# Kernel optimization log

Measured on AMD Instinct MI355X. Metric: run time of the kernel, lower is better.

Reference implementation:

```python
import math
import jax, jax.numpy as jnp
import numpy as np

T, B, IN, H, D, ETA, R = 128, 32, 512, 8, 64, 4, 4
DE = ETA * D  # expanded key dim = eta * head_dim
EPS = 1e-05


def setup_inputs() -> dict:
    key = jax.random.key(0)
    ks = jax.random.split(key, 8)
    s = 0.05
    return {
        "inputs": jax.random.normal(ks[0], (T, B, IN), jnp.float32),
        "terminations": jnp.zeros((T, B), jnp.float32),
        "tilde_k_prev": jax.random.normal(ks[1], (B, R, H, DE), jnp.float32) * s,
        "tilde_v_prev": jax.random.normal(ks[2], (B, R, H, D), jnp.float32) * s,
        "s_prev": jax.random.normal(ks[3], (B, H, DE), jnp.float32) * s,
        "tick": jnp.zeros((B, 1), jnp.float32),
        "W_kqv": jax.random.normal(ks[4], (H * D * 5, IN), jnp.float32) * s,
        "b_kqv": jnp.zeros((H * D * 5,), jnp.float32),
        "W_p": jax.random.normal(ks[5], (H * ETA * 3, IN), jnp.float32) * s,
        "b_p": jnp.zeros((H * ETA * 3,), jnp.float32),
        "W_o": jax.random.normal(ks[6], (IN, H * D), jnp.float32) * s,
        "b_o": jnp.zeros((IN,), jnp.float32),
    }


def _forward(inputs, terminations, tilde_k_prev, tilde_v_prev, s_prev, tick,
             W_kqv, b_kqv, W_p, b_p, W_o, b_o):
    # projections
    kqv = (inputs @ W_kqv.T + b_kqv).reshape(T, B, H, 5, D)
    keys, queries, values, beta, gammas = (kqv[..., i, :] for i in range(5))
    p = (inputs @ W_p.T + b_p).reshape(T, B, H, 3, ETA)
    p1, p2, p3 = (p[..., i, :] for i in range(3))
    relu, sig = jax.nn.relu, jax.nn.sigmoid
    # kernel feature maps: outer product then flatten (d outer, n inner)
    keys = jnp.einsum('tbhd,tbhn->tbhdn', relu(keys), relu(p1)).reshape(T, B, H, DE)
    queries = jnp.einsum('tbhd,tbhn->tbhdn', relu(queries), relu(p2)).reshape(T, B, H, DE)
    gammas = jnp.einsum('tbhd,tbhn->tbhdn', sig(gammas), sig(p3)).reshape(T, B, H, DE)
    beta = sig(beta)  # (T,B,H,D)
    # oscillatory basis
    ticks = tick[None] + jnp.arange(1, T + 1, dtype=jnp.float32).reshape(T, 1, 1)  # (T,B,1)
    omegas = jnp.linspace(-math.pi, math.pi, R)
    occil = jnp.cos(ticks * omegas[None, None, :])  # (T,B,R)
    values = values * beta
    values_r = values[:, :, None] * occil[:, :, :, None, None]   # (T,B,R,H,D)
    keys_g = keys * gammas                                        # (T,B,H,DE)
    keys_r = keys_g[:, :, None] * occil[:, :, :, None, None]     # (T,B,R,H,DE)
    # discounts (with termination resets)
    nt = (1.0 - terminations)[:, :, None, None]
    dg = (1.0 - gammas) * nt  # (T,B,H,DE)
    db = (1.0 - beta) * nt    # (T,B,H,D)
    # recurrence y[t] = discount[t]*y[t-1] + x[t] via lax.scan over T
    def step(carry, xs):
        k_st, v_st, s_st = carry
        kx, vx, sx, dgt, dbt = xs
        k_new = dgt[:, None] * k_st + kx   # (B,R,H,DE)
        v_new = dbt[:, None] * v_st + vx   # (B,R,H,D)
        s_new = dgt * s_st + sx            # (B,H,DE)
        return (k_new, v_new, s_new), (k_new, v_new, s_new)
    (kf, vf, sf), (K, V, S) = jax.lax.scan(
        step, (tilde_k_prev, tilde_v_prev, s_prev), (keys_r, values_r, keys_g, dg, db))
    # attention readout
    kdq = jnp.einsum('tbrhd,tbhd->tbrh', K, queries)
    kv = jnp.einsum('tbrhd,tbrh->tbhd', V, kdq)
    norm = jnp.einsum('tbhd,tbhd->tbh', S, queries)
    attn = kv / (2 * R * norm[..., None] + EPS)  # (T,B,H,D)
    out = attn.reshape(T, B, H * D) @ W_o.T + b_o  # dropout p=0 (eval)
    return out, kf, vf, sf, tick + T


def reference(inputs, terminations, tilde_k_prev, tilde_v_prev, s_prev, tick,
              W_kqv, b_kqv, W_p, b_p, W_o, b_o):
    return _forward(inputs, terminations, tilde_k_prev, tilde_v_prev, s_prev, tick,
                    W_kqv, b_kqv, W_p, b_p, W_o, b_o)
```

## Files before the change

kernel.cpp:

```cpp
#include <hip/hip_runtime.h>
#include <math.h>
#include <stdint.h>

constexpr int T_ = 128, B_ = 32, IN_ = 512, H_ = 8, D_ = 64, ETA_ = 4, R_ = 4;
constexpr int DE_ = ETA_ * D_;
constexpr float EPS_ = 1e-5f;
constexpr int M_   = T_ * B_;
constexpr int BH_  = B_ * H_;
constexpr int NC2  = 16;
constexpr int CH2  = T_ / NC2;

constexpr int NW = 2688;
constexpr int SPLITCOL = 1664;

typedef __attribute__((ext_vector_type(8))) short bf16x8;
typedef __attribute__((ext_vector_type(4))) float f32x4;

__device__ __forceinline__ float bf2f(unsigned short u) {
    return __builtin_bit_cast(float, ((unsigned)u) << 16);
}
__device__ __forceinline__ unsigned short f2bf(float f) {
    unsigned u = __builtin_bit_cast(unsigned, f);
    u = (u + 0x7fffu + ((u >> 16) & 1u)) >> 16;
    return (unsigned short)u;
}
__device__ __forceinline__ float fsigm(float x) {
    return __fdividef(1.f, 1.f + __expf(-x));
}

constexpr int N4A = M_ * 128;
constexpr int N4W = NW * 128;
constexpr int N8O = IN_ * IN_ / 8;
constexpr int NPREP = N4A + N4W + N8O;

__global__ __launch_bounds__(256) void prep_all(
    const float* __restrict__ inputs,
    const float* __restrict__ Wkqv, const float* __restrict__ Wp,
    const float* __restrict__ bkqv, const float* __restrict__ bp,
    const float* __restrict__ Wo,
    unsigned short* __restrict__ A2, unsigned short* __restrict__ W2,
    float* __restrict__ bias_perm, unsigned short* __restrict__ Wo_bf)
{
    int i = blockIdx.x * 256 + threadIdx.x;
    if (i < N4A) {
        const int r = i >> 7;
        const int c = (i & 127) << 2;
        float4 x = *(const float4*)(inputs + (size_t)r * 512 + c);
        ushort4 hi = make_ushort4(f2bf(x.x), f2bf(x.y), f2bf(x.z), f2bf(x.w));
        ushort4 lo = make_ushort4(f2bf(x.x - bf2f(hi.x)), f2bf(x.y - bf2f(hi.y)),
                                  f2bf(x.z - bf2f(hi.z)), f2bf(x.w - bf2f(hi.w)));
        unsigned short* dr = A2 + (size_t)r * 1024 + c;
        *(ushort4*)dr = hi;
        *(ushort4*)(dr + 512) = lo;
        return;
    }
    i -= N4A;
    if (i < N4W) {
        const int rr = i >> 7;
        const int c = (i & 127) << 2;
        bool zero = false;
        const float* srow = nullptr;
        float bv = 0.f;
        if (rr < 512) {
            const int h = rr >> 6, dd = rr & 63, s = h * 320 + dd;
            srow = Wkqv + (size_t)s * 512; bv = bkqv[s];
        } else if (rr < 1024) {
            const int q = rr - 512, h = q >> 6, dd = q & 63, s = h * 320 + 64 + dd;
            srow = Wkqv + (size_t)s * 512; bv = bkqv[s];
        } else if (rr < 1536) {
            const int q = rr - 1024, h = q >> 6, dd = q & 63, s = h * 320 + 256 + dd;
            srow = Wkqv + (size_t)s * 512; bv = bkqv[s];
        } else if (rr < 1632) {
            const int q = rr - 1536;
            srow = Wp + (size_t)q * 512; bv = bp[q];
        } else if (rr < 1664) {
            zero = true;
        } else if (rr < 2176) {
            const int q = rr - 1664, h = q >> 6, dd = q & 63, s = h * 320 + 128 + dd;
            srow = Wkqv + (size_t)s * 512; bv = bkqv[s];
        } else {
            const int q = rr - 2176, h = q >> 6, dd = q & 63, s = h * 320 + 192 + dd;
            srow = Wkqv + (size_t)s * 512; bv = bkqv[s];
        }
        float4 x = zero ? make_float4(0.f, 0.f, 0.f, 0.f) : *(const float4*)(srow + c);
        ushort4 hi = make_ushort4(f2bf(x.x), f2bf(x.y), f2bf(x.z), f2bf(x.w));
        ushort4 lo = make_ushort4(f2bf(x.x - bf2f(hi.x)), f2bf(x.y - bf2f(hi.y)),
                                  f2bf(x.z - bf2f(hi.z)), f2bf(x.w - bf2f(hi.w)));
        unsigned short* dr = W2 + (size_t)rr * 1536 + c;
        *(ushort4*)dr = hi;
        *(ushort4*)(dr + 512) = lo;
        *(ushort4*)(dr + 1024) = hi;
        if (c == 0) bias_perm[rr] = zero ? 0.f : bv;
        return;
    }
    i -= N4W;
    if (i < N8O) {
        const float4* s = (const float4*)Wo;
        float4 a = s[2 * i], b = s[2 * i + 1];
        *(ushort4*)(Wo_bf + 8 * i)     = make_ushort4(f2bf(a.x), f2bf(a.y), f2bf(a.z), f2bf(a.w));
        *(ushort4*)(Wo_bf + 8 * i + 4) = make_ushort4(f2bf(b.x), f2bf(b.y), f2bf(b.z), f2bf(b.w));
    }
}

__device__ __forceinline__ void gl_lds16(const unsigned short* g, unsigned short* l) {
    __builtin_amdgcn_global_load_lds((const __attribute__((address_space(1))) void*)g,
                                     (__attribute__((address_space(3))) void*)l, 16, 0, 0);
}

template <int BM, int BN>
__global__ __launch_bounds__(256) void gemm_bf16(
    const unsigned short* __restrict__ A,
    const unsigned short* __restrict__ W,
    const float* __restrict__ bias,
    float* __restrict__ C,
    int N, int sA, int sW, int kBig, int kSmall, int splitcol)
{
    constexpr int WM = BM / 2, WN = BN / 2;
    constexpr int AM = WM / 16, AN = WN / 16;
    constexpr int NLA = BM / 64;
    constexpr int NLB = BN / 64;
    constexpr int NLD = NLA + NLB;

    int bx, by;
    {
        const int nwg = gridDim.x * gridDim.y;
        int lin = blockIdx.y * gridDim.x + blockIdx.x;
        lin = (lin & 7) * (nwg >> 3) + (lin >> 3);
        const int G = (gridDim.x % 7 == 0) ? 7 : gridDim.x;
        const int grpsz = gridDim.y * G;
        const int cg = lin / grpsz, rem = lin % grpsz;
        by = rem / G;
        bx = cg * G + rem % G;
    }
    const int bm = by * BM;
    const int bn = bx * BN;
    const int tid = threadIdx.x;
    const int lane = tid & 63;
    const int wid = tid >> 6;
    const int wr = wid >> 1;
    const int wc = wid & 1;

    __shared__ __align__(16) unsigned short As[3][BM * 32];
    __shared__ __align__(16) unsigned short Bs[3][BN * 32];

    const unsigned short* aRow = A + (size_t)(bm + (tid & (BM - 1))) * sA
                                   + (tid / BM) * 8;
    const unsigned short* bRow = W + (size_t)(bn + (tid & (BN - 1))) * sW
                                   + (tid / BN) * 8;

    const int fA = (((lane >> 4) * BM) + wr * WM + (lane & 15)) * 8;
    const int fB = (((lane >> 4) * BN) + wc * WN + (lane & 15)) * 8;

    f32x4 acc[AM][AN] = {};
    const int K = (bn < splitcol) ? kBig : kSmall;
    const int NKT = K >> 5;

    auto stage = [&](int buf, int k0) {
        const int koA = (k0 >= 512) ? k0 - 512 : k0;
#pragma unroll
        for (int i = 0; i < NLA; ++i)
            gl_lds16(aRow + koA + i * (256 / BM) * 8,
                     &As[buf][(i * 256 + wid * 64) * 8]);
#pragma unroll
        for (int i = 0; i < NLB; ++i)
            gl_lds16(bRow + k0 + i * (256 / BN) * 8,
                     &Bs[buf][(i * 256 + wid * 64) * 8]);
    };

    stage(0, 0);
    if (NKT > 1) stage(1, 32);

    for (int kt = 0; kt < NKT; ++kt) {
        const int cur = kt % 3;
        if (kt + 2 < NKT) {
            stage((kt + 2) % 3, (kt + 2) << 5);
            if constexpr (NLD == 4)      asm volatile("s_waitcnt vmcnt(8)\ns_barrier" ::: "memory");
            else if constexpr (NLD == 3) asm volatile("s_waitcnt vmcnt(6)\ns_barrier" ::: "memory");
            else                         asm volatile("s_waitcnt vmcnt(4)\ns_barrier" ::: "memory");
        } else if (kt + 2 == NKT) {
            if constexpr (NLD == 4)      asm volatile("s_waitcnt vmcnt(4)\ns_barrier" ::: "memory");
            else if constexpr (NLD == 3) asm volatile("s_waitcnt vmcnt(3)\ns_barrier" ::: "memory");
            else                         asm volatile("s_waitcnt vmcnt(2)\ns_barrier" ::: "memory");
        } else {
            asm volatile("s_waitcnt vmcnt(0)\ns_barrier" ::: "memory");
        }
        __builtin_amdgcn_sched_barrier(0);

        bf16x8 af[AM], bfr[AN];
#pragma unroll
        for (int m = 0; m < AM; ++m) af[m] = *(const bf16x8*)&As[cur][fA + m * 128];
#pragma unroll
        for (int n = 0; n < AN; ++n) bfr[n] = *(const bf16x8*)&Bs[cur][fB + n * 128];
#pragma unroll
        for (int m = 0; m < AM; ++m)
#pragma unroll
            for (int n = 0; n < AN; ++n)
                acc[m][n] = __builtin_amdgcn_mfma_f32_16x16x32_bf16(af[m], bfr[n], acc[m][n], 0, 0, 0);

        asm volatile("s_waitcnt lgkmcnt(0)\ns_barrier" ::: "memory");
    }

#pragma unroll
    for (int n = 0; n < AN; ++n) {
        const int col = bn + wc * WN + n * 16 + (lane & 15);
        const float bv = bias[col];
#pragma unroll
        for (int m = 0; m < AM; ++m) {
            const int row0 = bm + wr * WM + m * 16 + ((lane >> 4) << 2);
#pragma unroll
            for (int j = 0; j < 4; ++j)
                C[(size_t)(row0 + j) * N + col] = acc[m][n][j] + bv;
        }
    }
}

template <int CTRL, int RM>
__device__ __forceinline__ float dpp_radd(float x) {
    int t = __builtin_amdgcn_update_dpp(0, __builtin_bit_cast(int, x), CTRL, RM, 0xf, true);
    return x + __builtin_bit_cast(float, t);
}
__device__ __forceinline__ float wave_allsum(float x) {
    x = dpp_radd<0x111, 0xf>(x);
    x = dpp_radd<0x112, 0xf>(x);
    x = dpp_radd<0x114, 0xf>(x);
    x = dpp_radd<0x118, 0xf>(x);
    x = dpp_radd<0x142, 0xa>(x);
    x = dpp_radd<0x143, 0xc>(x);
    return __builtin_bit_cast(float, __builtin_amdgcn_readlane(__builtin_bit_cast(int, x), 63));
}

__device__ __forceinline__ void osc2(float tt, float& oc03, float& oc12) {
    oc03 = cosf(3.14159265358979323846f * tt);
    oc12 = cosf(1.04719755119659774615f * tt);
}

__global__ __launch_bounds__(1024) void scan_fused(
    const float* __restrict__ kqv, const float* __restrict__ term,
    const float* __restrict__ tick,
    const float* __restrict__ k_prev, const float* __restrict__ v_prev,
    const float* __restrict__ s_prev,
    unsigned short* __restrict__ attn,
    float* __restrict__ kf, float* __restrict__ vf, float* __restrict__ sf,
    float* __restrict__ tick_out)
{
    const int bh = blockIdx.x;
    const int b = bh >> 3, h = bh & 7;
    const int tid = threadIdx.x;
    const int w = tid >> 6;
    const int d = tid & 63;

    __shared__ float LK[NC2][4][DE_];
    __shared__ float LS[NC2][DE_];
    __shared__ float LV[NC2][4][D_];
    __shared__ float LDg[NC2][DE_];
    __shared__ float LDb[NC2][D_];

    const float tk = tick[b];

    float K0[4] = {}, K1[4] = {}, K2[4] = {}, K3[4] = {}, S[4] = {};
    float V0 = 0.f, V1 = 0.f, V2 = 0.f, V3 = 0.f;
    float Dgv[4] = {1.f, 1.f, 1.f, 1.f};
    float Dbv = 1.f;

    if (w == 0) {
        float4 k4;
        k4 = *(const float4*)&k_prev[((size_t)(b * 4 + 0) * 8 + h) * DE_ + 4 * d];
        K0[0] = k4.x; K0[1] = k4.y; K0[2] = k4.z; K0[3] = k4.w;
        k4 = *(const float4*)&k_prev[((size_t)(b * 4 + 1) * 8 + h) * DE_ + 4 * d];
        K1[0] = k4.x; K1[1] = k4.y; K1[2] = k4.z; K1[3] = k4.w;
        k4 = *(const float4*)&k_prev[((size_t)(b * 4 + 2) * 8 + h) * DE_ + 4 * d];
        K2[0] = k4.x; K2[1] = k4.y; K2[2] = k4.z; K2[3] = k4.w;
        k4 = *(const float4*)&k_prev[((size_t)(b * 4 + 3) * 8 + h) * DE_ + 4 * d];
        K3[0] = k4.x; K3[1] = k4.y; K3[2] = k4.z; K3[3] = k4.w;
        k4 = *(const float4*)&s_prev[((size_t)b * 8 + h) * DE_ + 4 * d];
        S[0] = k4.x; S[1] = k4.y; S[2] = k4.z; S[3] = k4.w;
        V0 = v_prev[((size_t)(b * 4 + 0) * 8 + h) * D_ + d];
        V1 = v_prev[((size_t)(b * 4 + 1) * 8 + h) * D_ + d];
        V2 = v_prev[((size_t)(b * 4 + 2) * 8 + h) * D_ + d];
        V3 = v_prev[((size_t)(b * 4 + 3) * 8 + h) * D_ + d];
    }

#pragma unroll 4
    for (int tt = 0; tt < CH2; ++tt) {
        const int t = w * CH2 + tt;
        const float* row = kqv + ((size_t)t * B_ + b) * NW;
        const float c0 = row[h * 64 + d];
        const float c2 = row[1664 + h * 64 + d];
        const float c3 = row[2176 + h * 64 + d];
        const float c4 = row[1024 + h * 64 + d];
        const float* pr = row + 1536 + h * 12;
        const float4 p1 = *(const float4*)pr;
        const float4 p3 = *(const float4*)(pr + 8);
        const float nt = 1.f - term[(size_t)t * B_ + b];

        float oc03, oc12; osc2(tk + (float)(t + 1), oc03, oc12);
        const float sgam = fsigm(c4);
        const float rk = fmaxf(c0, 0.f);
        const float sbet = fsigm(c3);
        const float vb = c2 * sbet;
        const float dbv = (1.f - sbet) * nt;
        const float p1a[4] = {p1.x, p1.y, p1.z, p1.w};
        const float p3a[4] = {p3.x, p3.y, p3.z, p3.w};
#pragma unroll
        for (int n = 0; n < 4; ++n) {
            const float g  = sgam * fsigm(p3a[n]);
            const float kg = rk * fmaxf(p1a[n], 0.f) * g;
            const float dg = (1.f - g) * nt;
            S[n]  = fmaf(dg, S[n],  kg);
            K0[n] = fmaf(dg, K0[n], kg * oc03);
            K1[n] = fmaf(dg, K1[n], kg * oc12);
            K2[n] = fmaf(dg, K2[n], kg * oc12);
            K3[n] = fmaf(dg, K3[n], kg * oc03);
            Dgv[n] *= dg;
        }
        V0 = fmaf(dbv, V0, vb * oc03);
        V1 = fmaf(dbv, V1, vb * oc12);
        V2 = fmaf(dbv, V2, vb * oc12);
        V3 = fmaf(dbv, V3, vb * oc03);
        Dbv *= dbv;
    }

    *(float4*)&LK[w][0][4 * d] = make_float4(K0[0], K0[1], K0[2], K0[3]);
    *(float4*)&LK[w][1][4 * d] = make_float4(K1[0], K1[1], K1[2], K1[3]);
    *(float4*)&LK[w][2][4 * d] = make_float4(K2[0], K2[1], K2[2], K2[3]);
    *(float4*)&LK[w][3][4 * d] = make_float4(K3[0], K3[1], K3[2], K3[3]);
    *(float4*)&LS[w][4 * d]    = make_float4(S[0], S[1], S[2], S[3]);
    LV[w][0][d] = V0; LV[w][1][d] = V1; LV[w][2][d] = V2; LV[w][3][d] = V3;
    *(float4*)&LDg[w][4 * d]   = make_float4(Dgv[0], Dgv[1], Dgv[2], Dgv[3]);
    LDb[w][d] = Dbv;
    __syncthreads();

    if (tid < DE_) {
        const int de = tid;
        float c0 = LK[0][0][de], c1k = LK[0][1][de], c2k = LK[0][2][de],
              c3k = LK[0][3][de], cs = LS[0][de];
        for (int c = 1; c < NC2; ++c) {
            const float dg = LDg[c][de];
            float n0 = fmaf(dg, c0,  LK[c][0][de]); LK[c][0][de] = c0;  c0  = n0;
            float n1 = fmaf(dg, c1k, LK[c][1][de]); LK[c][1][de] = c1k; c1k = n1;
            float n2 = fmaf(dg, c2k, LK[c][2][de]); LK[c][2][de] = c2k; c2k = n2;
            float n3 = fmaf(dg, c3k, LK[c][3][de]); LK[c][3][de] = c3k; c3k = n3;
            float ns = fmaf(dg, cs,  LS[c][de]);    LS[c][de]    = cs;  cs  = ns;
        }
        kf[((size_t)(b * 4 + 0) * 8 + h) * DE_ + de] = c0;
        kf[((size_t)(b * 4 + 1) * 8 + h) * DE_ + de] = c1k;
        kf[((size_t)(b * 4 + 2) * 8 + h) * DE_ + de] = c2k;
        kf[((size_t)(b * 4 + 3) * 8 + h) * DE_ + de] = c3k;
        sf[((size_t)b * 8 + h) * DE_ + de] = cs;
    } else if (tid < DE_ + D_) {
        const int dd = tid - DE_;
        float v0 = LV[0][0][dd], v1 = LV[0][1][dd], v2 = LV[0][2][dd], v3 = LV[0][3][dd];
        for (int c = 1; c < NC2; ++c) {
            const float db = LDb[c][dd];
            float n0 = fmaf(db, v0, LV[c][0][dd]); LV[c][0][dd] = v0; v0 = n0;
            float n1 = fmaf(db, v1, LV[c][1][dd]); LV[c][1][dd] = v1; v1 = n1;
            float n2 = fmaf(db, v2, LV[c][2][dd]); LV[c][2][dd] = v2; v2 = n2;
            float n3 = fmaf(db, v3, LV[c][3][dd]); LV[c][3][dd] = v3; v3 = n3;
        }
        vf[((size_t)(b * 4 + 0) * 8 + h) * D_ + dd] = v0;
        vf[((size_t)(b * 4 + 1) * 8 + h) * D_ + dd] = v1;
        vf[((size_t)(b * 4 + 2) * 8 + h) * D_ + dd] = v2;
        vf[((size_t)(b * 4 + 3) * 8 + h) * D_ + dd] = v3;
    }
    if (h == 0 && tid == 0) tick_out[b] = tk + (float)T_;
    __syncthreads();

    if (w == 0) {
        float4 k4;
        k4 = *(const float4*)&k_prev[((size_t)(b * 4 + 0) * 8 + h) * DE_ + 4 * d];
        K0[0] = k4.x; K0[1] = k4.y; K0[2] = k4.z; K0[3] = k4.w;
        k4 = *(const float4*)&k_prev[((size_t)(b * 4 + 1) * 8 + h) * DE_ + 4 * d];
        K1[0] = k4.x; K1[1] = k4.y; K1[2] = k4.z; K1[3] = k4.w;
        k4 = *(const float4*)&k_prev[((size_t)(b * 4 + 2) * 8 + h) * DE_ + 4 * d];
        K2[0] = k4.x; K2[1] = k4.y; K2[2] = k4.z; K2[3] = k4.w;
        k4 = *(const float4*)&k_prev[((size_t)(b * 4 + 3) * 8 + h) * DE_ + 4 * d];
        K3[0] = k4.x; K3[1] = k4.y; K3[2] = k4.z; K3[3] = k4.w;
        k4 = *(const float4*)&s_prev[((size_t)b * 8 + h) * DE_ + 4 * d];
        S[0] = k4.x; S[1] = k4.y; S[2] = k4.z; S[3] = k4.w;
        V0 = v_prev[((size_t)(b * 4 + 0) * 8 + h) * D_ + d];
        V1 = v_prev[((size_t)(b * 4 + 1) * 8 + h) * D_ + d];
        V2 = v_prev[((size_t)(b * 4 + 2) * 8 + h) * D_ + d];
        V3 = v_prev[((size_t)(b * 4 + 3) * 8 + h) * D_ + d];
    } else {
        float4 k4;
        k4 = *(const float4*)&LK[w][0][4 * d];
        K0[0] = k4.x; K0[1] = k4.y; K0[2] = k4.z; K0[3] = k4.w;
        k4 = *(const float4*)&LK[w][1][4 * d];
        K1[0] = k4.x; K1[1] = k4.y; K1[2] = k4.z; K1[3] = k4.w;
        k4 = *(const float4*)&LK[w][2][4 * d];
        K2[0] = k4.x; K2[1] = k4.y; K2[2] = k4.z; K2[3] = k4.w;
        k4 = *(const float4*)&LK[w][3][4 * d];
        K3[0] = k4.x; K3[1] = k4.y; K3[2] = k4.z; K3[3] = k4.w;
        k4 = *(const float4*)&LS[w][4 * d];
        S[0] = k4.x; S[1] = k4.y; S[2] = k4.z; S[3] = k4.w;
        V0 = LV[w][0][d]; V1 = LV[w][1][d]; V2 = LV[w][2][d]; V3 = LV[w][3][d];
    }

#pragma unroll 4
    for (int tt = 0; tt < CH2; ++tt) {
        const int t = w * CH2 + tt;
        const float* row = kqv + ((size_t)t * B_ + b) * NW;
        const float c0 = row[h * 64 + d];
        const float c1 = row[512 + h * 64 + d];
        const float c2 = row[1664 + h * 64 + d];
        const float c3 = row[2176 + h * 64 + d];
        const float c4 = row[1024 + h * 64 + d];
        const float* pr = row + 1536 + h * 12;
        const float4 p1 = *(const float4*)pr;
        const float4 p2 = *(const float4*)(pr + 4);
        const float4 p3 = *(const float4*)(pr + 8);
        const float nt = 1.f - term[(size_t)t * B_ + b];

        float oc03, oc12; osc2(tk + (float)(t + 1), oc03, oc12);
        const float sgam = fsigm(c4);
        const float rk = fmaxf(c0, 0.f);
        const float rq = fmaxf(c1, 0.f);
        const float sbet = fsigm(c3);
        const float vb = c2 * sbet;
        const float dbv = (1.f - sbet) * nt;
        const float p1a[4] = {p1.x, p1.y, p1.z, p1.w};
        const float p2a[4] = {p2.x, p2.y, p2.z, p2.w};
        const float p3a[4] = {p3.x, p3.y, p3.z, p3.w};

        float s0 = 0.f, s1 = 0.f, s2 = 0.f, s3 = 0.f, s4 = 0.f;
#pragma unroll
        for (int n = 0; n < 4; ++n) {
            const float g  = sgam * fsigm(p3a[n]);
            const float kg = rk * fmaxf(p1a[n], 0.f) * g;
            const float qe = rq * fmaxf(p2a[n], 0.f);
            const float dg = (1.f - g) * nt;
            S[n]  = fmaf(dg, S[n],  kg);
            K0[n] = fmaf(dg, K0[n], kg * oc03);
            K1[n] = fmaf(dg, K1[n], kg * oc12);
            K2[n] = fmaf(dg, K2[n], kg * oc12);
            K3[n] = fmaf(dg, K3[n], kg * oc03);
            s0 = fmaf(K0[n], qe, s0);
            s1 = fmaf(K1[n], qe, s1);
            s2 = fmaf(K2[n], qe, s2);
            s3 = fmaf(K3[n], qe, s3);
            s4 = fmaf(S[n],  qe, s4);
        }
        V0 = fmaf(dbv, V0, vb * oc03);
        V1 = fmaf(dbv, V1, vb * oc12);
        V2 = fmaf(dbv, V2, vb * oc12);
        V3 = fmaf(dbv, V3, vb * oc03);

        const float kdq0 = wave_allsum(s0);
        const float kdq1 = wave_allsum(s1);
        const float kdq2 = wave_allsum(s2);
        const float kdq3 = wave_allsum(s3);
        const float nrm  = wave_allsum(s4);

        const float kv = V0 * kdq0 + V1 * kdq1 + V2 * kdq2 + V3 * kdq3;
        attn[((size_t)t * B_ + b) * (H_ * D_) + h * D_ + d] =
            f2bf(__fdividef(kv, 2.f * (float)R_ * nrm + EPS_));
    }
}

extern "C" void kernel_launch(void* const* d_in, const int* in_sizes, int n_in,
                              void* d_out, int out_size, void* d_ws, size_t ws_size,
                              hipStream_t stream)
{
    const float* inputs = (const float*)d_in[0];
    const float* term   = (const float*)d_in[1];
    const float* k_prev = (const float*)d_in[2];
    const float* v_prev = (const float*)d_in[3];
    const float* s_prev = (const float*)d_in[4];
    const float* tick   = (const float*)d_in[5];
    const float* W_kqv  = (const float*)d_in[6];
    const float* b_kqv  = (const float*)d_in[7];
    const float* W_p    = (const float*)d_in[8];
    const float* b_p    = (const float*)d_in[9];
    const float* W_o    = (const float*)d_in[10];
    const float* b_o    = (const float*)d_in[11];

    float* out = (float*)d_out;
    float* kf  = out + (size_t)T_ * B_ * IN_;
    float* vf  = kf  + (size_t)B_ * R_ * H_ * DE_;
    float* sf  = vf  + (size_t)B_ * R_ * H_ * D_;
    float* tick_out = sf + (size_t)B_ * H_ * DE_;

    float* kqv_s = (float*)d_ws;
    unsigned short* attn_bf = (unsigned short*)(kqv_s + (size_t)M_ * NW);
    unsigned short* Wo_bf   = attn_bf + (size_t)M_ * IN_;
    unsigned short* A2      = Wo_bf + (size_t)IN_ * (H_ * D_);
    unsigned short* W2      = A2 + (size_t)M_ * 1024;
    float* bias_perm        = (float*)(W2 + (size_t)NW * 1536);

    prep_all<<<(NPREP + 255) / 256, 256, 0, stream>>>(
        inputs, W_kqv, W_p, b_kqv, b_p, W_o, A2, W2, bias_perm, Wo_bf);

    {
        dim3 grid(NW / 128, M_ / 128);
        gemm_bf16<128, 128><<<grid, 256, 0, stream>>>(A2, W2, bias_perm, kqv_s,
                                                      NW, 1024, 1536, 1536, 512, SPLITCOL);
    }

    scan_fused<<<BH_, 1024, 0, stream>>>(kqv_s, term, tick, k_prev, v_prev, s_prev,
                                         attn_bf, kf, vf, sf, tick_out);

    {
        dim3 grid(IN_ / 64, M_ / 64);
        gemm_bf16<64, 64><<<grid, 256, 0, stream>>>(attn_bf, Wo_bf, b_o, out,
                                                    IN_, 512, 512, 512, 512, 0);
    }
}
```

Baseline: 139.5 us.

## Split the 3-pass split-bf16 projection GEMM into separate K-slices with atomic accumulation

The high-precision columns of the projection GEMM previously ran a single K=1536 loop over hi/lo/hi bf16 passes. They now launch as three separate K=512 work-groups that atomically add into an output buffer pre-filled with bias by the prep kernel. This evens out per-block work and raises the grid size, but adds fp32 atomics and extra bias-init traffic. The GEMM pipeline also drops from a 3-stage buffer with hand-tuned vmcnt waits to a simpler 2-stage double buffer with __syncthreads, which may expose more load latency.

```diff
diff --git a/kernel.cpp b/kernel.cpp
--- a/kernel.cpp
+++ b/kernel.cpp
@@ -11,7 +11,8 @@
 constexpr int CH2  = T_ / NC2;
 
 constexpr int NW = 2688;
-constexpr int SPLITCOL = 1664;
+constexpr int NBIG = 13;
+constexpr int NCOL = NW / 128;
 
 typedef __attribute__((ext_vector_type(8))) short bf16x8;
 typedef __attribute__((ext_vector_type(4))) float f32x4;
@@ -28,10 +29,21 @@
     return __fdividef(1.f, 1.f + __expf(-x));
 }
 
+__device__ __forceinline__ float bias_decode(
+    int col, const float* __restrict__ bkqv, const float* __restrict__ bp)
+{
+    if (col < 512)  return bkqv[(col >> 6) * 320 + (col & 63)];
+    if (col < 1024) { int q = col - 512;  return bkqv[(q >> 6) * 320 + 64 + (q & 63)]; }
+    if (col < 1536) { int q = col - 1024; return bkqv[(q >> 6) * 320 + 256 + (q & 63)]; }
+    if (col < 1632) return bp[col - 1536];
+    return 0.f;
+}
+
 constexpr int N4A = M_ * 128;
 constexpr int N4W = NW * 128;
 constexpr int N8O = IN_ * IN_ / 8;
-constexpr int NPREP = N4A + N4W + N8O;
+constexpr int NIT = M_ * (1664 / 4);
+constexpr int NPREP = N4A + N4W + N8O + NIT;
 
 __global__ __launch_bounds__(256) void prep_all(
     const float* __restrict__ inputs,
@@ -39,7 +51,8 @@
     const float* __restrict__ bkqv, const float* __restrict__ bp,
     const float* __restrict__ Wo,
     unsigned short* __restrict__ A2, unsigned short* __restrict__ W2,
-    float* __restrict__ bias_perm, unsigned short* __restrict__ Wo_bf)
+    float* __restrict__ bias_perm, unsigned short* __restrict__ Wo_bf,
+    float* __restrict__ kqv_s)
 {
     int i = blockIdx.x * 256 + threadIdx.x;
     if (i < N4A) {
@@ -86,10 +99,9 @@
         ushort4 hi = make_ushort4(f2bf(x.x), f2bf(x.y), f2bf(x.z), f2bf(x.w));
         ushort4 lo = make_ushort4(f2bf(x.x - bf2f(hi.x)), f2bf(x.y - bf2f(hi.y)),
                                   f2bf(x.z - bf2f(hi.z)), f2bf(x.w - bf2f(hi.w)));
-        unsigned short* dr = W2 + (size_t)rr * 1536 + c;
+        unsigned short* dr = W2 + (size_t)rr * 1024 + c;
         *(ushort4*)dr = hi;
         *(ushort4*)(dr + 512) = lo;
-        *(ushort4*)(dr + 1024) = hi;
         if (c == 0) bias_perm[rr] = zero ? 0.f : bv;
         return;
     }
@@ -99,6 +111,15 @@
         float4 a = s[2 * i], b = s[2 * i + 1];
         *(ushort4*)(Wo_bf + 8 * i)     = make_ushort4(f2bf(a.x), f2bf(a.y), f2bf(a.z), f2bf(a.w));
         *(ushort4*)(Wo_bf + 8 * i + 4) = make_ushort4(f2bf(b.x), f2bf(b.y), f2bf(b.z), f2bf(b.w));
+        return;
+    }
+    i -= N8O;
+    if (i < NIT) {
+        const int r = i / 416;
+        const int c = (i % 416) * 4;
+        *(float4*)(kqv_s + (size_t)r * NW + c) =
+            make_float4(bias_decode(c, bkqv, bp), bias_decode(c + 1, bkqv, bp),
+                        bias_decode(c + 2, bkqv, bp), bias_decode(c + 3, bkqv, bp));
     }
 }
 
@@ -107,19 +128,18 @@
                                      (__attribute__((address_space(3))) void*)l, 16, 0, 0);
 }
 
-template <int BM, int BN>
+template <int BM, int BN, bool SPLITK>
 __global__ __launch_bounds__(256) void gemm_bf16(
     const unsigned short* __restrict__ A,
     const unsigned short* __restrict__ W,
     const float* __restrict__ bias,
     float* __restrict__ C,
-    int N, int sA, int sW, int kBig, int kSmall, int splitcol)
+    int N, int sA, int sW, int K)
 {
     constexpr int WM = BM / 2, WN = BN / 2;
     constexpr int AM = WM / 16, AN = WN / 16;
     constexpr int NLA = BM / 64;
     constexpr int NLB = BN / 64;
-    constexpr int NLD = NLA + NLB;
 
     int bx, by;
     {
@@ -132,34 +152,46 @@
         by = rem / G;
         bx = cg * G + rem % G;
     }
+    int bn, koA = 0, koB = 0;
+    bool atom = false;
+    if constexpr (SPLITK) {
+        if (bx < 3 * NBIG) {
+            const int pass = bx / NBIG;
+            bn = (bx % NBIG) * BN;
+            koA = (pass == 2) ? 512 : 0;
+            koB = (pass == 1) ? 512 : 0;
+            atom = true;
+        } else {
+            bn = (NBIG + bx - 3 * NBIG) * BN;
+        }
+    } else {
+        bn = bx * BN;
+    }
     const int bm = by * BM;
-    const int bn = bx * BN;
     const int tid = threadIdx.x;
     const int lane = tid & 63;
     const int wid = tid >> 6;
     const int wr = wid >> 1;
     const int wc = wid & 1;
 
-    __shared__ __align__(16) unsigned short As[3][BM * 32];
-    __shared__ __align__(16) unsigned short Bs[3][BN * 32];
+    __shared__ __align__(16) unsigned short As[2][BM * 32];
+    __shared__ __align__(16) unsigned short Bs[2][BN * 32];
 
     const unsigned short* aRow = A + (size_t)(bm + (tid & (BM - 1))) * sA
-                                   + (tid / BM) * 8;
+                                   + (tid / BM) * 8 + koA;
     const unsigned short* bRow = W + (size_t)(bn + (tid & (BN - 1))) * sW
-                                   + (tid / BN) * 8;
+                                   + (tid / BN) * 8 + koB;
 
     const int fA = (((lane >> 4) * BM) + wr * WM + (lane & 15)) * 8;
     const int fB = (((lane >> 4) * BN) + wc * WN + (lane & 15)) * 8;
 
     f32x4 acc[AM][AN] = {};
-    const int K = (bn < splitcol) ? kBig : kSmall;
     const int NKT = K >> 5;
 
     auto stage = [&](int buf, int k0) {
-        const int koA = (k0 >= 512) ? k0 - 512 : k0;
 #pragma unroll
         for (int i = 0; i < NLA; ++i)
-            gl_lds16(aRow + koA + i * (256 / BM) * 8,
+            gl_lds16(aRow + k0 + i * (256 / BM) * 8,
                      &As[buf][(i * 256 + wid * 64) * 8]);
 #pragma unroll
         for (int i = 0; i < NLB; ++i)
@@ -168,24 +200,11 @@
     };
 
     stage(0, 0);
-    if (NKT > 1) stage(1, 32);
+    __syncthreads();
 
     for (int kt = 0; kt < NKT; ++kt) {
-        const int cur = kt % 3;
-        if (kt + 2 < NKT) {
-            stage((kt + 2) % 3, (kt + 2) << 5);
-            if constexpr (NLD == 4)      asm volatile("s_waitcnt vmcnt(8)\ns_barrier" ::: "memory");
-            else if constexpr (NLD == 3) asm volatile("s_waitcnt vmcnt(6)\ns_barrier" ::: "memory");
-            else                         asm volatile("s_waitcnt vmcnt(4)\ns_barrier" ::: "memory");
-        } else if (kt + 2 == NKT) {
-            if constexpr (NLD == 4)      asm volatile("s_waitcnt vmcnt(4)\ns_barrier" ::: "memory");
-            else if constexpr (NLD == 3) asm volatile("s_waitcnt vmcnt(3)\ns_barrier" ::: "memory");
-            else                         asm volatile("s_waitcnt vmcnt(2)\ns_barrier" ::: "memory");
-        } else {
-            asm volatile("s_waitcnt vmcnt(0)\ns_barrier" ::: "memory");
-        }
-        __builtin_amdgcn_sched_barrier(0);
-
+        const int cur = kt & 1;
+        if (kt + 1 < NKT) stage(cur ^ 1, (kt + 1) << 5);
         bf16x8 af[AM], bfr[AN];
 #pragma unroll
         for (int m = 0; m < AM; ++m) af[m] = *(const bf16x8*)&As[cur][fA + m * 128];
@@ -196,8 +215,7 @@
 #pragma unroll
             for (int n = 0; n < AN; ++n)
                 acc[m][n] = __builtin_amdgcn_mfma_f32_16x16x32_bf16(af[m], bfr[n], acc[m][n], 0, 0, 0);
-
-        asm volatile("s_waitcnt lgkmcnt(0)\ns_barrier" ::: "memory");
+        __syncthreads();
     }
 
 #pragma unroll
@@ -208,8 +226,11 @@
         for (int m = 0; m < AM; ++m) {
             const int row0 = bm + wr * WM + m * 16 + ((lane >> 4) << 2);
 #pragma unroll
-            for (int j = 0; j < 4; ++j)
-                C[(size_t)(row0 + j) * N + col] = acc[m][n][j] + bv;
+            for (int j = 0; j < 4; ++j) {
+                const size_t idx = (size_t)(row0 + j) * N + col;
+                if (atom) atomicAdd(&C[idx], acc[m][n][j]);
+                else      C[idx] = acc[m][n][j] + bv;
+            }
         }
     }
 }
@@ -485,15 +506,15 @@
     unsigned short* Wo_bf   = attn_bf + (size_t)M_ * IN_;
     unsigned short* A2      = Wo_bf + (size_t)IN_ * (H_ * D_);
     unsigned short* W2      = A2 + (size_t)M_ * 1024;
-    float* bias_perm        = (float*)(W2 + (size_t)NW * 1536);
+    float* bias_perm        = (float*)(W2 + (size_t)NW * 1024);
 
     prep_all<<<(NPREP + 255) / 256, 256, 0, stream>>>(
-        inputs, W_kqv, W_p, b_kqv, b_p, W_o, A2, W2, bias_perm, Wo_bf);
+        inputs, W_kqv, W_p, b_kqv, b_p, W_o, A2, W2, bias_perm, Wo_bf, kqv_s);
 
     {
-        dim3 grid(NW / 128, M_ / 128);
-        gemm_bf16<128, 128><<<grid, 256, 0, stream>>>(A2, W2, bias_perm, kqv_s,
-                                                      NW, 1024, 1536, 1536, 512, SPLITCOL);
+        dim3 grid(3 * NBIG + (NCOL - NBIG), M_ / 128);
+        gemm_bf16<128, 128, true><<<grid, 256, 0, stream>>>(
+            A2, W2, bias_perm, kqv_s, NW, 1024, 1024, 512);
     }
 
     scan_fused<<<BH_, 1024, 0, stream>>>(kqv_s, term, tick, k_prev, v_prev, s_prev,
@@ -501,7 +522,7 @@
 
     {
         dim3 grid(IN_ / 64, M_ / 64);
-        gemm_bf16<64, 64><<<grid, 256, 0, stream>>>(attn_bf, Wo_bf, b_o, out,
-                                                    IN_, 512, 512, 512, 512, 0);
-    }
-}
+        gemm_bf16<64, 64, false><<<grid, 256, 0, stream>>>(
+            attn_bf, Wo_bf, b_o, out, IN_, 512, 512, 512);
+    }
+}
```

Result: slower. 175.0 us (+25.4%).
